# Optimization experiments

Measured on AMD Instinct MI355X. Metric: run time of the kernel, lower is better.

## Reference

```python
import jax, jax.numpy as jnp
import numpy as np

NC = 80
REG_MAX = 16
NO = REG_MAX * 4 + NC  # 144
LEVEL_SHAPES = [(80, 80), (40, 40), (20, 20)]
STRIDES = [8.0, 16.0, 32.0]
CHANNELS = [256, 512, 512]


def _make_anchors():
    """Returns anchor_points (2, A) and stride_tensor (1, A), grid offset 0.5."""
    pts, sts = [], []
    for (h, w), s in zip(LEVEL_SHAPES, STRIDES):
        sx = jnp.arange(w, dtype=jnp.float32) + 0.5
        sy = jnp.arange(h, dtype=jnp.float32) + 0.5
        gy, gx = jnp.meshgrid(sy, sx, indexing='ij')
        pts.append(jnp.stack([gx.ravel(), gy.ravel()], axis=-1))  # (h*w, 2)
        sts.append(jnp.full((h * w,), s, dtype=jnp.float32))
    anchors = jnp.concatenate(pts, axis=0).T          # (2, A)
    strides = jnp.concatenate(sts, axis=0)[None, :]   # (1, A)
    return anchors, strides


def setup_inputs() -> dict:
    key = jax.random.key(0)
    ks = jax.random.split(key, 16)
    inp = {}
    inp['x0'] = jax.random.normal(ks[0], (16, 256, 80, 80), dtype=jnp.float32)
    inp['x1'] = jax.random.normal(ks[1], (16, 512, 40, 40), dtype=jnp.float32)
    inp['x2'] = jax.random.normal(ks[2], (16, 512, 20, 20), dtype=jnp.float32)
    # per-level 1x1 conv head weights: box branch (4*reg_max out), cls branch (nc out)
    for i, c in enumerate(CHANNELS):
        sc = 1.0 / np.sqrt(c)
        inp[f'w_box{i}'] = jax.random.normal(ks[3 + 4 * i], (REG_MAX * 4, c), dtype=jnp.float32) * sc
        inp[f'b_box{i}'] = jax.random.normal(ks[4 + 4 * i], (REG_MAX * 4,), dtype=jnp.float32) * 0.01
        inp[f'w_cls{i}'] = jax.random.normal(ks[5 + 4 * i], (NC, c), dtype=jnp.float32) * sc
        inp[f'b_cls{i}'] = jax.random.normal(ks[6 + 4 * i], (NC,), dtype=jnp.float32) * 0.01
    return inp


def _level_out(x, wb, bb, wc, bc):
    # cat(cv2(x), cv3(x), dim=1) then view(B, no, -1)
    box = jnp.einsum('bchw,oc->bohw', x, wb) + bb[None, :, None, None]
    cls = jnp.einsum('bchw,oc->bohw', x, wc) + bc[None, :, None, None]
    B = x.shape[0]
    return jnp.concatenate([box, cls], axis=1).reshape(B, NO, -1)


def reference(x0, x1, x2,
              w_box0, b_box0, w_cls0, b_cls0,
              w_box1, b_box1, w_cls1, b_cls1,
              w_box2, b_box2, w_cls2, b_cls2):
    xs = [x0, x1, x2]
    wbs = [w_box0, w_box1, w_box2]
    bbs = [b_box0, b_box1, b_box2]
    wcs = [w_cls0, w_cls1, w_cls2]
    bcs = [b_cls0, b_cls1, b_cls2]
    x_cat = jnp.concatenate(
        [_level_out(x, wb, bb, wc, bc) for x, wb, bb, wc, bc in zip(xs, wbs, bbs, wcs, bcs)],
        axis=2)  # (B, 144, A)
    B, _, A = x_cat.shape
    box, cls = x_cat[:, :REG_MAX * 4, :], x_cat[:, REG_MAX * 4:, :]

    # DFL: (B, 4*16, A) -> softmax over 16 bins -> expected distance per side
    p = jax.nn.softmax(box.reshape(B, 4, REG_MAX, A), axis=2)
    dist = jnp.einsum('bkra,r->bka', p, jnp.arange(REG_MAX, dtype=jnp.float32))  # (B, 4, A)

    # dist2bbox (xywh) on anchor grid, scale by stride
    anchors, strides = _make_anchors()
    anc = anchors[None]                 # (1, 2, A)
    lt, rb = dist[:, :2, :], dist[:, 2:, :]
    x1y1 = anc - lt
    x2y2 = anc + rb
    c_xy = (x1y1 + x2y2) * 0.5
    wh = x2y2 - x1y1
    dbox = jnp.concatenate([c_xy, wh], axis=1) * strides[:, None, :]  # (B, 4, A)

    # boxes (B, A, 4), scores (B, A, nc) -- the tensors fed to EfficientNMS_TRT
    boxes = jnp.transpose(dbox, (0, 2, 1))
    scores = jnp.transpose(cls, (0, 2, 1))
    return jnp.concatenate([boxes, scores], axis=-1)  # (B, A, 4 + nc)
```

## Files before the change

### kernel.cpp

```cpp
#include <hip/hip_runtime.h>


typedef __bf16 bf16x8 __attribute__((ext_vector_type(8)));
typedef float  f32x4  __attribute__((ext_vector_type(4)));

#define NTHREADS 256

#define WCHUNK 9216
#define WOFF0 0
#define WOFF1 73728
#define WOFF2 221184

__device__ __forceinline__ unsigned int pack_bf16(float a, float b) {
    unsigned int ua = __builtin_bit_cast(unsigned int, a);
    unsigned int ub = __builtin_bit_cast(unsigned int, b);
    return ((ua + 0x8000u) >> 16) | ((ub + 0x8000u) & 0xffff0000u);
}

__device__ __forceinline__ int swz32(int row, int kbyte) {
    return row * 64 + (kbyte ^ ((((row & 3) ^ ((row >> 2) & 1))) << 4));
}

__device__ __forceinline__ void gload_lds16(const void* g, void* l) {
    __builtin_amdgcn_global_load_lds(
        (const __attribute__((address_space(1))) void*)g,
        (__attribute__((address_space(3))) void*)l, 16, 0, 0);
}

__global__ __launch_bounds__(256)
void prep_w_kernel(const float* __restrict__ wb0, const float* __restrict__ wc0,
                   const float* __restrict__ wb1, const float* __restrict__ wc1,
                   const float* __restrict__ wb2, const float* __restrict__ wc2,
                   unsigned char* __restrict__ ws) {
    int uid = blockIdx.x * 256 + threadIdx.x;
    if (uid >= 23040) return;
    const float* wb; const float* wc; int C; size_t off; int uu;
    if (uid < 4608)       { wb = wb0; wc = wc0; C = 256; off = WOFF0; uu = uid; }
    else if (uid < 13824) { wb = wb1; wc = wc1; C = 512; off = WOFF1; uu = uid - 4608; }
    else                  { wb = wb2; wc = wc2; C = 512; off = WOFF2; uu = uid - 13824; }
    const int kunits = C / 8;
    const int row = uu / kunits;
    const int k   = (uu % kunits) * 8;
    const float* src = ((row < 64) ? (wb + row * C) : (wc + (row - 64) * C)) + k;
    const float4 f0 = *(const float4*)(src);
    const float4 f1 = *(const float4*)(src + 4);
    uint4 p;
    p.x = pack_bf16(f0.x, f0.y);
    p.y = pack_bf16(f0.z, f0.w);
    p.z = pack_bf16(f1.x, f1.y);
    p.w = pack_bf16(f1.z, f1.w);
    const int chunk = k >> 5;
    const int kg    = (k & 31) >> 3;
    *(uint4*)(ws + off + (size_t)chunk * WCHUNK + swz32(row, kg * 16)) = p;
}

template <int LVL>
__device__ __forceinline__ void run_level(
        int rb,
        const float* __restrict__ x,
        const unsigned char* __restrict__ wimg_all,
        const float* __restrict__ bbox, const float* __restrict__ bcls,
        float* __restrict__ out,
        unsigned char* s_w) {

    constexpr int    C      = (LVL == 0) ? 256 : 512;
    constexpr int    GW     = (LVL == 0) ? 80 : (LVL == 1 ? 40 : 20);
    constexpr int    HW     = GW * GW;
    constexpr int    AOFF   = (LVL == 0) ? 0 : (LVL == 1 ? 6400 : 8000);
    constexpr float  STRIDE = (LVL == 0) ? 8.0f : (LVL == 1 ? 16.0f : 32.0f);
    constexpr int    TPB    = (HW + 127) / 128;
    constexpr size_t WOFF   = (LVL == 0) ? WOFF0 : (LVL == 1 ? WOFF1 : WOFF2);
    const int nkc = C / 32;

    const int b    = rb / TPB;
    const int tile = rb % TPB;
    const int hw0  = tile * 128;
    const int nv   = (HW - hw0 < 128) ? (HW - hw0) : 128;

    const int tid  = threadIdx.x;
    const int wv   = tid >> 6;
    const int lane = tid & 63;
    const int col  = lane & 15;
    const int q4   = lane >> 4;

    const float* xb = x + (size_t)b * C * HW;
    const unsigned char* wimg = wimg_all + WOFF;

    const int a0 = wv * 16 + col;
    const int a1 = 64 + a0;
    const int a0c = (a0 < nv) ? a0 : (nv - 1);
    const int a1c = (a1 < nv) ? a1 : (nv - 1);
    const float* xanc0 = xb + hw0 + a0c;
    const float* xanc1 = xb + hw0 + a1c;

    f32x4 acc[9][2];
#pragma unroll
    for (int m = 0; m < 9; ++m) {
        acc[m][0] = (f32x4){0.f, 0.f, 0.f, 0.f};
        acc[m][1] = (f32x4){0.f, 0.f, 0.f, 0.f};
    }

    float P[16];

#define XLOAD(CC)                                                           \
    {                                                                       \
        const size_t _kb = (size_t)((CC) * 32 + q4 * 8) * HW;               \
        const float* _p0 = xanc0 + _kb;                                     \
        const float* _p1 = xanc1 + _kb;                                     \
        _Pragma("unroll")                                                   \
        for (int _j = 0; _j < 8; ++_j) {                                    \
            P[_j]     = _p0[(size_t)_j * HW];                               \
            P[8 + _j] = _p1[(size_t)_j * HW];                               \
        }                                                                   \
    }

#define WDMA(CC, BUF)                                                       \
    {                                                                       \
        _Pragma("unroll")                                                   \
        for (int _i = 0; _i < 3; ++_i) {                                    \
            int _u = tid + _i * 256;                                        \
            if (_u < 576)                                                   \
                gload_lds16(wimg + (size_t)(CC) * WCHUNK + _u * 16,         \
                            s_w + (BUF) * WCHUNK + _u * 16);                \
        }                                                                   \
    }

#define CVT(O, DST)                                                         \
    {                                                                       \
        uint4 _q;                                                           \
        _q.x = pack_bf16(P[(O) + 0], P[(O) + 1]);                           \
        _q.y = pack_bf16(P[(O) + 2], P[(O) + 3]);                           \
        _q.z = pack_bf16(P[(O) + 4], P[(O) + 5]);                           \
        _q.w = pack_bf16(P[(O) + 6], P[(O) + 7]);                           \
        DST = __builtin_bit_cast(bf16x8, _q);                               \
    }

    WDMA(0, 0);
    XLOAD(0);
    __builtin_amdgcn_sched_barrier(0);
    asm volatile("s_waitcnt vmcnt(16)" ::: "memory");
    __builtin_amdgcn_s_barrier();
    __builtin_amdgcn_sched_barrier(0);

    for (int kc = 0; kc < nkc; ++kc) {
        const unsigned char* wb = s_w + (kc & 1) * WCHUNK;
        const bool more = (kc + 1 < nkc);

        if (more) WDMA(kc + 1, (kc & 1) ^ 1);

        bf16x8 fA, fB;
        CVT(0, fA);
        CVT(8, fB);

        if (more) XLOAD(kc + 1);
        __builtin_amdgcn_sched_barrier(0);

#pragma unroll
        for (int m = 0; m < 9; ++m) {
            const bf16x8 af = *(const bf16x8*)(wb + swz32(m * 16 + col, q4 * 16));
            acc[m][0] = __builtin_amdgcn_mfma_f32_16x16x32_bf16(af, fA, acc[m][0], 0, 0, 0);
            acc[m][1] = __builtin_amdgcn_mfma_f32_16x16x32_bf16(af, fB, acc[m][1], 0, 0, 0);
        }
        __builtin_amdgcn_sched_barrier(0);

        if (more) asm volatile("s_waitcnt vmcnt(16)" ::: "memory");
        else      asm volatile("s_waitcnt vmcnt(0)"  ::: "memory");
        __builtin_amdgcn_s_barrier();
        __builtin_amdgcn_sched_barrier(0);
    }

#undef CVT
#undef WDMA
#undef XLOAD

    float4 bcv[5];
#pragma unroll
    for (int m = 0; m < 5; ++m)
        bcv[m] = *(const float4*)(bcls + m * 16 + q4 * 4);

    const float LOG2E = 1.44269504088896f;

#pragma unroll
    for (int nf = 0; nf < 2; ++nf) {
        const int alocal = nf * 64 + wv * 16 + col;
        const bool valid = alocal < nv;
        const int hw = hw0 + alocal;

        float dist[4];
#pragma unroll
        for (int g = 0; g < 4; ++g) {
            const float4 bbv = *(const float4*)(bbox + g * 16 + q4 * 4);
            const float v0 = acc[g][nf][0] + bbv.x;
            const float v1 = acc[g][nf][1] + bbv.y;
            const float v2 = acc[g][nf][2] + bbv.z;
            const float v3 = acc[g][nf][3] + bbv.w;
            float mx = fmaxf(fmaxf(v0, v1), fmaxf(v2, v3));
            mx = fmaxf(mx, __shfl_xor(mx, 16));
            mx = fmaxf(mx, __shfl_xor(mx, 32));
            const float e0 = __builtin_amdgcn_exp2f((v0 - mx) * LOG2E);
            const float e1 = __builtin_amdgcn_exp2f((v1 - mx) * LOG2E);
            const float e2 = __builtin_amdgcn_exp2f((v2 - mx) * LOG2E);
            const float e3 = __builtin_amdgcn_exp2f((v3 - mx) * LOG2E);
            float s  = e0 + e1 + e2 + e3;
            float ws = e1 + 2.f * e2 + 3.f * e3 + (float)(q4 * 4) * s;
            s  += __shfl_xor(s, 16);
            s  += __shfl_xor(s, 32);
            ws += __shfl_xor(ws, 16);
            ws += __shfl_xor(ws, 32);
            dist[g] = ws / s;
        }

        if (valid) {
            const size_t obase = ((size_t)b * 8400 + AOFF + hw) * 84;
            if (q4 == 0) {
                const float ax = (float)(hw % GW) + 0.5f;
                const float ay = (float)(hw / GW) + 0.5f;
                f32x4 bx;
                bx[0] = (ax + 0.5f * (dist[2] - dist[0])) * STRIDE;
                bx[1] = (ay + 0.5f * (dist[3] - dist[1])) * STRIDE;
                bx[2] = (dist[0] + dist[2]) * STRIDE;
                bx[3] = (dist[1] + dist[3]) * STRIDE;
                *(f32x4*)(out + obase) = bx;
            }
#pragma unroll
            for (int m = 0; m < 5; ++m) {
                f32x4 v;
                v[0] = acc[m + 4][nf][0] + bcv[m].x;
                v[1] = acc[m + 4][nf][1] + bcv[m].y;
                v[2] = acc[m + 4][nf][2] + bcv[m].z;
                v[3] = acc[m + 4][nf][3] + bcv[m].w;
                *(f32x4*)(out + obase + 4 + m * 16 + q4 * 4) = v;
            }
        }
    }
}

__global__ __launch_bounds__(NTHREADS, 4)
void UltralyticsDetect_kernel(
        const float* __restrict__ x0, const float* __restrict__ x1, const float* __restrict__ x2,
        const unsigned char* __restrict__ wimg,
        const float* __restrict__ bb0, const float* __restrict__ bc0,
        const float* __restrict__ bb1, const float* __restrict__ bc1,
        const float* __restrict__ bb2, const float* __restrict__ bc2,
        float* __restrict__ out) {

    __shared__ __align__(16) unsigned char s_w[2 * WCHUNK];

    const int bid = blockIdx.x;
    if (bid < 208) {
        run_level<1>(bid, x1, wimg, bb1, bc1, out, s_w);
    } else if (bid < 272) {
        run_level<2>(bid - 208, x2, wimg, bb2, bc2, out, s_w);
    } else {
        run_level<0>(bid - 272, x0, wimg, bb0, bc0, out, s_w);
    }
}

extern "C" void kernel_launch(void* const* d_in, const int* in_sizes, int n_in,
                              void* d_out, int out_size, void* d_ws, size_t ws_size,
                              hipStream_t stream) {
    const float* x0  = (const float*)d_in[0];
    const float* x1  = (const float*)d_in[1];
    const float* x2  = (const float*)d_in[2];
    const float* wb0 = (const float*)d_in[3];
    const float* bb0 = (const float*)d_in[4];
    const float* wc0 = (const float*)d_in[5];
    const float* bc0 = (const float*)d_in[6];
    const float* wb1 = (const float*)d_in[7];
    const float* bb1 = (const float*)d_in[8];
    const float* wc1 = (const float*)d_in[9];
    const float* bc1 = (const float*)d_in[10];
    const float* wb2 = (const float*)d_in[11];
    const float* bb2 = (const float*)d_in[12];
    const float* wc2 = (const float*)d_in[13];
    const float* bc2 = (const float*)d_in[14];

    unsigned char* wimg = (unsigned char*)d_ws;

    prep_w_kernel<<<90, 256, 0, stream>>>(wb0, wc0, wb1, wc1, wb2, wc2, wimg);

    UltralyticsDetect_kernel<<<1072, NTHREADS, 0, stream>>>(
        x0, x1, x2, wimg,
        bb0, bc0, bb1, bc1, bb2, bc2,
        (float*)d_out);
}
```

Before: 51.11 us.

## Switch to single-wave blocks of 64 anchors with 4 MFMA column tiles per wave

Each block becomes one 64-thread wave that covers 64 anchors, using four 16-column MFMA tiles, where before four waves each covered 32 anchors of a 128-anchor tile. The whole weight chunk is DMA'd to LDS by that one wave, so the workgroup s_barrier calls are gone, and the grid roughly doubles to 2112 blocks. The cost is that every wave now loads the full 9 KB weight chunk into LDS per k-step, with no sharing across waves. Register pressure also rises from 72 to 144 accumulator floats and 32 staged inputs, and the occupancy hint drops.

```diff
diff --git a/kernel.cpp b/kernel.cpp
--- a/kernel.cpp
+++ b/kernel.cpp
@@ -3,8 +3,6 @@
 
 typedef __bf16 bf16x8 __attribute__((ext_vector_type(8)));
 typedef float  f32x4  __attribute__((ext_vector_type(4)));
-
-#define NTHREADS 256
 
 #define WCHUNK 9216
 #define WOFF0 0
@@ -68,60 +66,58 @@
     constexpr int    HW     = GW * GW;
     constexpr int    AOFF   = (LVL == 0) ? 0 : (LVL == 1 ? 6400 : 8000);
     constexpr float  STRIDE = (LVL == 0) ? 8.0f : (LVL == 1 ? 16.0f : 32.0f);
-    constexpr int    TPB    = (HW + 127) / 128;
+    constexpr int    TPB    = (HW + 63) / 64;
     constexpr size_t WOFF   = (LVL == 0) ? WOFF0 : (LVL == 1 ? WOFF1 : WOFF2);
     const int nkc = C / 32;
 
     const int b    = rb / TPB;
     const int tile = rb % TPB;
-    const int hw0  = tile * 128;
-    const int nv   = (HW - hw0 < 128) ? (HW - hw0) : 128;
-
-    const int tid  = threadIdx.x;
-    const int wv   = tid >> 6;
-    const int lane = tid & 63;
+    const int hw0  = tile * 64;
+    const int nv   = (HW - hw0 < 64) ? (HW - hw0) : 64;
+
+    const int lane = threadIdx.x;
     const int col  = lane & 15;
     const int q4   = lane >> 4;
 
-    const float* xb = x + (size_t)b * C * HW;
+    const float* xhw = x + (size_t)b * C * HW + hw0;
     const unsigned char* wimg = wimg_all + WOFF;
 
-    const int a0 = wv * 16 + col;
-    const int a1 = 64 + a0;
-    const int a0c = (a0 < nv) ? a0 : (nv - 1);
-    const int a1c = (a1 < nv) ? a1 : (nv - 1);
-    const float* xanc0 = xb + hw0 + a0c;
-    const float* xanc1 = xb + hw0 + a1c;
-
-    f32x4 acc[9][2];
-#pragma unroll
-    for (int m = 0; m < 9; ++m) {
-        acc[m][0] = (f32x4){0.f, 0.f, 0.f, 0.f};
-        acc[m][1] = (f32x4){0.f, 0.f, 0.f, 0.f};
-    }
-
-    float P[16];
+    int af[4];
+#pragma unroll
+    for (int f = 0; f < 4; ++f) {
+        const int a = f * 16 + col;
+        af[f] = (a < nv) ? a : (nv - 1);
+    }
+    const int q4ofs = q4 * 8 * HW;
+
+    f32x4 acc[9][4];
+#pragma unroll
+    for (int m = 0; m < 9; ++m)
+#pragma unroll
+        for (int f = 0; f < 4; ++f)
+            acc[m][f] = (f32x4){0.f, 0.f, 0.f, 0.f};
+
+    float P[32];
 
 #define XLOAD(CC)                                                           \
     {                                                                       \
-        const size_t _kb = (size_t)((CC) * 32 + q4 * 8) * HW;               \
-        const float* _p0 = xanc0 + _kb;                                     \
-        const float* _p1 = xanc1 + _kb;                                     \
+        const float* _pb = xhw + (size_t)(CC) * 32 * HW;                    \
         _Pragma("unroll")                                                   \
         for (int _j = 0; _j < 8; ++_j) {                                    \
-            P[_j]     = _p0[(size_t)_j * HW];                               \
-            P[8 + _j] = _p1[(size_t)_j * HW];                               \
+            const float* _p = _pb + (size_t)_j * HW + q4ofs;                \
+            _Pragma("unroll")                                               \
+            for (int _f = 0; _f < 4; ++_f)                                  \
+                P[_f * 8 + _j] = _p[af[_f]];                                \
         }                                                                   \
     }
 
 #define WDMA(CC, BUF)                                                       \
     {                                                                       \
         _Pragma("unroll")                                                   \
-        for (int _i = 0; _i < 3; ++_i) {                                    \
-            int _u = tid + _i * 256;                                        \
-            if (_u < 576)                                                   \
-                gload_lds16(wimg + (size_t)(CC) * WCHUNK + _u * 16,         \
-                            s_w + (BUF) * WCHUNK + _u * 16);                \
+        for (int _i = 0; _i < 9; ++_i) {                                    \
+            const int _u = lane + _i * 64;                                  \
+            gload_lds16(wimg + (size_t)(CC) * WCHUNK + _u * 16,             \
+                        s_w + (BUF) * WCHUNK + _u * 16);                    \
         }                                                                   \
     }
 
@@ -138,8 +134,7 @@
     WDMA(0, 0);
     XLOAD(0);
     __builtin_amdgcn_sched_barrier(0);
-    asm volatile("s_waitcnt vmcnt(16)" ::: "memory");
-    __builtin_amdgcn_s_barrier();
+    asm volatile("s_waitcnt vmcnt(32)" ::: "memory");
     __builtin_amdgcn_sched_barrier(0);
 
     for (int kc = 0; kc < nkc; ++kc) {
@@ -147,25 +142,28 @@
         const bool more = (kc + 1 < nkc);
 
         if (more) WDMA(kc + 1, (kc & 1) ^ 1);
-
-        bf16x8 fA, fB;
-        CVT(0, fA);
-        CVT(8, fB);
+        __builtin_amdgcn_sched_barrier(0);
+
+        bf16x8 f0, f1, f2, f3;
+        CVT(0, f0);
+        CVT(8, f1);
+        CVT(16, f2);
+        CVT(24, f3);
 
         if (more) XLOAD(kc + 1);
         __builtin_amdgcn_sched_barrier(0);
 
 #pragma unroll
         for (int m = 0; m < 9; ++m) {
-            const bf16x8 af = *(const bf16x8*)(wb + swz32(m * 16 + col, q4 * 16));
-            acc[m][0] = __builtin_amdgcn_mfma_f32_16x16x32_bf16(af, fA, acc[m][0], 0, 0, 0);
-            acc[m][1] = __builtin_amdgcn_mfma_f32_16x16x32_bf16(af, fB, acc[m][1], 0, 0, 0);
+            const bf16x8 a_ = *(const bf16x8*)(wb + swz32(m * 16 + col, q4 * 16));
+            acc[m][0] = __builtin_amdgcn_mfma_f32_16x16x32_bf16(a_, f0, acc[m][0], 0, 0, 0);
+            acc[m][1] = __builtin_amdgcn_mfma_f32_16x16x32_bf16(a_, f1, acc[m][1], 0, 0, 0);
+            acc[m][2] = __builtin_amdgcn_mfma_f32_16x16x32_bf16(a_, f2, acc[m][2], 0, 0, 0);
+            acc[m][3] = __builtin_amdgcn_mfma_f32_16x16x32_bf16(a_, f3, acc[m][3], 0, 0, 0);
         }
         __builtin_amdgcn_sched_barrier(0);
 
-        if (more) asm volatile("s_waitcnt vmcnt(16)" ::: "memory");
-        else      asm volatile("s_waitcnt vmcnt(0)"  ::: "memory");
-        __builtin_amdgcn_s_barrier();
+        if (more) asm volatile("s_waitcnt vmcnt(32)" ::: "memory");
         __builtin_amdgcn_sched_barrier(0);
     }
 
@@ -181,8 +179,8 @@
     const float LOG2E = 1.44269504088896f;
 
 #pragma unroll
-    for (int nf = 0; nf < 2; ++nf) {
-        const int alocal = nf * 64 + wv * 16 + col;
+    for (int nf = 0; nf < 4; ++nf) {
+        const int alocal = nf * 16 + col;
         const bool valid = alocal < nv;
         const int hw = hw0 + alocal;
 
@@ -235,7 +233,7 @@
     }
 }
 
-__global__ __launch_bounds__(NTHREADS, 4)
+__global__ __launch_bounds__(64, 2)
 void UltralyticsDetect_kernel(
         const float* __restrict__ x0, const float* __restrict__ x1, const float* __restrict__ x2,
         const unsigned char* __restrict__ wimg,
@@ -247,12 +245,12 @@
     __shared__ __align__(16) unsigned char s_w[2 * WCHUNK];
 
     const int bid = blockIdx.x;
-    if (bid < 208) {
+    if (bid < 400) {
         run_level<1>(bid, x1, wimg, bb1, bc1, out, s_w);
-    } else if (bid < 272) {
-        run_level<2>(bid - 208, x2, wimg, bb2, bc2, out, s_w);
+    } else if (bid < 512) {
+        run_level<2>(bid - 400, x2, wimg, bb2, bc2, out, s_w);
     } else {
-        run_level<0>(bid - 272, x0, wimg, bb0, bc0, out, s_w);
+        run_level<0>(bid - 512, x0, wimg, bb0, bc0, out, s_w);
     }
 }
 
@@ -279,7 +277,7 @@
 
     prep_w_kernel<<<90, 256, 0, stream>>>(wb0, wc0, wb1, wc1, wb2, wc2, wimg);
 
-    UltralyticsDetect_kernel<<<1072, NTHREADS, 0, stream>>>(
+    UltralyticsDetect_kernel<<<2112, 64, 0, stream>>>(
         x0, x1, x2, wimg,
         bb0, bc0, bb1, bc1, bb2, bc2,
         (float*)d_out);
```

Result: faster. 49.96 us (-2.3%).

## Stage activation tiles through LDS via direct global-to-LDS DMA with swizzle

Applied to the files above, without the earlier changes.

Activation loads change from per-thread strided scalar global loads into registers to 16-byte global_load_lds DMA of 32-channel by 128-anchor tiles into a double-buffered, XOR-swizzled LDS buffer. Threads then read their fragments from LDS and convert them to bf16. This is meant to replace the poorly coalesced scalar gathers with wide contiguous transfers. Tail tiles are shifted to overlap the previous tile rather than masked, so some anchors are computed and written twice. LDS grows by 32 KB per block, launch bounds drop to 3 blocks per CU, and the pipeline now waits for vmcnt(0) each iteration.

```diff
diff --git a/kernel.cpp b/kernel.cpp
--- a/kernel.cpp
+++ b/kernel.cpp
@@ -10,6 +10,8 @@
 #define WOFF0 0
 #define WOFF1 73728
 #define WOFF2 221184
+
+#define XBUF 16384
 
 __device__ __forceinline__ unsigned int pack_bf16(float a, float b) {
     unsigned int ua = __builtin_bit_cast(unsigned int, a);
@@ -61,7 +63,7 @@
         const unsigned char* __restrict__ wimg_all,
         const float* __restrict__ bbox, const float* __restrict__ bcls,
         float* __restrict__ out,
-        unsigned char* s_w) {
+        unsigned char* s_w, unsigned char* s_x) {
 
     constexpr int    C      = (LVL == 0) ? 256 : 512;
     constexpr int    GW     = (LVL == 0) ? 80 : (LVL == 1 ? 40 : 20);
@@ -74,8 +76,8 @@
 
     const int b    = rb / TPB;
     const int tile = rb % TPB;
-    const int hw0  = tile * 128;
-    const int nv   = (HW - hw0 < 128) ? (HW - hw0) : 128;
+    int hw0 = tile * 128;
+    if (hw0 > HW - 128) hw0 = HW - 128;
 
     const int tid  = threadIdx.x;
     const int wv   = tid >> 6;
@@ -83,15 +85,13 @@
     const int col  = lane & 15;
     const int q4   = lane >> 4;
 
-    const float* xb = x + (size_t)b * C * HW;
+    const float* xlev = x + (size_t)b * C * HW;
     const unsigned char* wimg = wimg_all + WOFF;
 
-    const int a0 = wv * 16 + col;
-    const int a1 = 64 + a0;
-    const int a0c = (a0 < nv) ? a0 : (nv - 1);
-    const int a1c = (a1 < nv) ? a1 : (nv - 1);
-    const float* xanc0 = xb + hw0 + a0c;
-    const float* xanc1 = xb + hw0 + a1c;
+    const int xg  = (((lane & 31) ^ (wv << 2)) << 2);
+    const int xr  = lane >> 5;
+    const int xrd0 = (((wv * 32 + col) << 2) ^ (q4 << 6)) + q4 * 8 * 512;
+    const int xrd1 = (((wv * 32 + 16 + col) << 2) ^ (q4 << 6)) + q4 * 8 * 512;
 
     f32x4 acc[9][2];
 #pragma unroll
@@ -100,17 +100,13 @@
         acc[m][1] = (f32x4){0.f, 0.f, 0.f, 0.f};
     }
 
-    float P[16];
-
-#define XLOAD(CC)                                                           \
+#define XDMA(CC, BUF)                                                       \
     {                                                                       \
-        const size_t _kb = (size_t)((CC) * 32 + q4 * 8) * HW;               \
-        const float* _p0 = xanc0 + _kb;                                     \
-        const float* _p1 = xanc1 + _kb;                                     \
         _Pragma("unroll")                                                   \
-        for (int _j = 0; _j < 8; ++_j) {                                    \
-            P[_j]     = _p0[(size_t)_j * HW];                               \
-            P[8 + _j] = _p1[(size_t)_j * HW];                               \
+        for (int _i = 0; _i < 4; ++_i) {                                    \
+            const int _r2 = wv * 8 + _i * 2;                                \
+            gload_lds16(xlev + (size_t)((CC) * 32 + _r2 + xr) * HW + hw0 + xg, \
+                        s_x + (BUF) * XBUF + _r2 * 512);                    \
         }                                                                   \
     }
 
@@ -118,60 +114,63 @@
     {                                                                       \
         _Pragma("unroll")                                                   \
         for (int _i = 0; _i < 3; ++_i) {                                    \
-            int _u = tid + _i * 256;                                        \
+            const int _u = tid + _i * 256;                                  \
             if (_u < 576)                                                   \
                 gload_lds16(wimg + (size_t)(CC) * WCHUNK + _u * 16,         \
                             s_w + (BUF) * WCHUNK + _u * 16);                \
         }                                                                   \
     }
 
-#define CVT(O, DST)                                                         \
-    {                                                                       \
-        uint4 _q;                                                           \
-        _q.x = pack_bf16(P[(O) + 0], P[(O) + 1]);                           \
-        _q.y = pack_bf16(P[(O) + 2], P[(O) + 3]);                           \
-        _q.z = pack_bf16(P[(O) + 4], P[(O) + 5]);                           \
-        _q.w = pack_bf16(P[(O) + 6], P[(O) + 7]);                           \
-        DST = __builtin_bit_cast(bf16x8, _q);                               \
-    }
-
+    XDMA(0, 0);
     WDMA(0, 0);
-    XLOAD(0);
     __builtin_amdgcn_sched_barrier(0);
-    asm volatile("s_waitcnt vmcnt(16)" ::: "memory");
+    asm volatile("s_waitcnt vmcnt(0)" ::: "memory");
     __builtin_amdgcn_s_barrier();
     __builtin_amdgcn_sched_barrier(0);
 
     for (int kc = 0; kc < nkc; ++kc) {
-        const unsigned char* wb = s_w + (kc & 1) * WCHUNK;
+        const int cur = kc & 1;
         const bool more = (kc + 1 < nkc);
 
-        if (more) WDMA(kc + 1, (kc & 1) ^ 1);
-
-        bf16x8 fA, fB;
-        CVT(0, fA);
-        CVT(8, fB);
-
-        if (more) XLOAD(kc + 1);
+        if (more) {
+            XDMA(kc + 1, cur ^ 1);
+            WDMA(kc + 1, cur ^ 1);
+        }
         __builtin_amdgcn_sched_barrier(0);
 
+        const unsigned char* xbuf = s_x + cur * XBUF;
+        float xf0[8], xf1[8];
+#pragma unroll
+        for (int j = 0; j < 8; ++j) {
+            xf0[j] = *(const float*)(xbuf + xrd0 + j * 512);
+            xf1[j] = *(const float*)(xbuf + xrd1 + j * 512);
+        }
+        uint4 qa, qb;
+        qa.x = pack_bf16(xf0[0], xf0[1]); qa.y = pack_bf16(xf0[2], xf0[3]);
+        qa.z = pack_bf16(xf0[4], xf0[5]); qa.w = pack_bf16(xf0[6], xf0[7]);
+        qb.x = pack_bf16(xf1[0], xf1[1]); qb.y = pack_bf16(xf1[2], xf1[3]);
+        qb.z = pack_bf16(xf1[4], xf1[5]); qb.w = pack_bf16(xf1[6], xf1[7]);
+        const bf16x8 fA = __builtin_bit_cast(bf16x8, qa);
+        const bf16x8 fB = __builtin_bit_cast(bf16x8, qb);
+
+        const unsigned char* wbuf = s_w + cur * WCHUNK;
 #pragma unroll
         for (int m = 0; m < 9; ++m) {
-            const bf16x8 af = *(const bf16x8*)(wb + swz32(m * 16 + col, q4 * 16));
-            acc[m][0] = __builtin_amdgcn_mfma_f32_16x16x32_bf16(af, fA, acc[m][0], 0, 0, 0);
-            acc[m][1] = __builtin_amdgcn_mfma_f32_16x16x32_bf16(af, fB, acc[m][1], 0, 0, 0);
+            const bf16x8 a_ = *(const bf16x8*)(wbuf + swz32(m * 16 + col, q4 * 16));
+            acc[m][0] = __builtin_amdgcn_mfma_f32_16x16x32_bf16(a_, fA, acc[m][0], 0, 0, 0);
+            acc[m][1] = __builtin_amdgcn_mfma_f32_16x16x32_bf16(a_, fB, acc[m][1], 0, 0, 0);
         }
         __builtin_amdgcn_sched_barrier(0);
 
-        if (more) asm volatile("s_waitcnt vmcnt(16)" ::: "memory");
-        else      asm volatile("s_waitcnt vmcnt(0)"  ::: "memory");
-        __builtin_amdgcn_s_barrier();
-        __builtin_amdgcn_sched_barrier(0);
-    }
-
-#undef CVT
+        if (more) {
+            asm volatile("s_waitcnt vmcnt(0)" ::: "memory");
+            __builtin_amdgcn_s_barrier();
+            __builtin_amdgcn_sched_barrier(0);
+        }
+    }
+
 #undef WDMA
-#undef XLOAD
+#undef XDMA
 
     float4 bcv[5];
 #pragma unroll
@@ -182,8 +181,7 @@
 
 #pragma unroll
     for (int nf = 0; nf < 2; ++nf) {
-        const int alocal = nf * 64 + wv * 16 + col;
-        const bool valid = alocal < nv;
+        const int alocal = wv * 32 + nf * 16 + col;
         const int hw = hw0 + alocal;
 
         float dist[4];
@@ -210,32 +208,30 @@
             dist[g] = ws / s;
         }
 
-        if (valid) {
-            const size_t obase = ((size_t)b * 8400 + AOFF + hw) * 84;
-            if (q4 == 0) {
-                const float ax = (float)(hw % GW) + 0.5f;
-                const float ay = (float)(hw / GW) + 0.5f;
-                f32x4 bx;
-                bx[0] = (ax + 0.5f * (dist[2] - dist[0])) * STRIDE;
-                bx[1] = (ay + 0.5f * (dist[3] - dist[1])) * STRIDE;
-                bx[2] = (dist[0] + dist[2]) * STRIDE;
-                bx[3] = (dist[1] + dist[3]) * STRIDE;
-                *(f32x4*)(out + obase) = bx;
-            }
-#pragma unroll
-            for (int m = 0; m < 5; ++m) {
-                f32x4 v;
-                v[0] = acc[m + 4][nf][0] + bcv[m].x;
-                v[1] = acc[m + 4][nf][1] + bcv[m].y;
-                v[2] = acc[m + 4][nf][2] + bcv[m].z;
-                v[3] = acc[m + 4][nf][3] + bcv[m].w;
-                *(f32x4*)(out + obase + 4 + m * 16 + q4 * 4) = v;
-            }
-        }
-    }
-}
-
-__global__ __launch_bounds__(NTHREADS, 4)
+        const size_t obase = ((size_t)b * 8400 + AOFF + hw) * 84;
+        if (q4 == 0) {
+            const float ax = (float)(hw % GW) + 0.5f;
+            const float ay = (float)(hw / GW) + 0.5f;
+            f32x4 bx;
+            bx[0] = (ax + 0.5f * (dist[2] - dist[0])) * STRIDE;
+            bx[1] = (ay + 0.5f * (dist[3] - dist[1])) * STRIDE;
+            bx[2] = (dist[0] + dist[2]) * STRIDE;
+            bx[3] = (dist[1] + dist[3]) * STRIDE;
+            *(f32x4*)(out + obase) = bx;
+        }
+#pragma unroll
+        for (int m = 0; m < 5; ++m) {
+            f32x4 v;
+            v[0] = acc[m + 4][nf][0] + bcv[m].x;
+            v[1] = acc[m + 4][nf][1] + bcv[m].y;
+            v[2] = acc[m + 4][nf][2] + bcv[m].z;
+            v[3] = acc[m + 4][nf][3] + bcv[m].w;
+            *(f32x4*)(out + obase + 4 + m * 16 + q4 * 4) = v;
+        }
+    }
+}
+
+__global__ __launch_bounds__(NTHREADS, 3)
 void UltralyticsDetect_kernel(
         const float* __restrict__ x0, const float* __restrict__ x1, const float* __restrict__ x2,
         const unsigned char* __restrict__ wimg,
@@ -245,14 +241,15 @@
         float* __restrict__ out) {
 
     __shared__ __align__(16) unsigned char s_w[2 * WCHUNK];
+    __shared__ __align__(16) unsigned char s_x[2 * XBUF];
 
     const int bid = blockIdx.x;
     if (bid < 208) {
-        run_level<1>(bid, x1, wimg, bb1, bc1, out, s_w);
+        run_level<1>(bid, x1, wimg, bb1, bc1, out, s_w, s_x);
     } else if (bid < 272) {
-        run_level<2>(bid - 208, x2, wimg, bb2, bc2, out, s_w);
+        run_level<2>(bid - 208, x2, wimg, bb2, bc2, out, s_w, s_x);
     } else {
-        run_level<0>(bid - 272, x0, wimg, bb0, bc0, out, s_w);
+        run_level<0>(bid - 272, x0, wimg, bb0, bc0, out, s_w, s_x);
     }
 }
 
```

Result: faster. 48.30 us (median of 2 runs) (-5.5%).
